# Kernel tuning notes

Measured on AMD Instinct MI355X. Metric: run time of the kernel, lower is better.

## Reference

```python
import jax, jax.numpy as jnp
import numpy as np
from jax import lax

B, C, H, W = 16, 3, 256, 256
K = 3          # lbp kernel size (odd)
POOL = 2
Q = 8          # quant_len
LN_EPS = 1e-5


def _lbp_kernel(c, k):
    half = k // 2
    idx_pairs = [[[0, 0], [k - 1, k - 1]],
                 [[0, half], [k - 1, half]],
                 [[0, k - 1], [k - 1, 0]],
                 [[half, k - 1], [half, 0]]]
    kerns = []
    for pair in idx_pairs:
        for idx in pair:
            m = np.zeros((c, k, k), np.float32)
            m[:, half, half] = 1.0
            m[:, idx[0], idx[1]] = -1.0
            kerns.append(m)
    return jnp.asarray(np.stack(kerns))  # [8, C, K, K]


LBP_KERNEL = _lbp_kernel(C, K)


def setup_inputs() -> dict:
    key = jax.random.key(0)
    ks = jax.random.split(key, 8)
    return {
        "x": jax.random.normal(ks[0], (B, C, H, W), jnp.float32),
        "clamp_low": jnp.float32(-150.0),
        "clamp_high": jnp.float32(150.0),
        "w_expand": jax.random.normal(ks[1], (56, 3, 1, 1), jnp.float32) * 0.1,
        "b_expand": jax.random.normal(ks[2], (56,), jnp.float32) * 0.05,
        "w_conv": jax.random.normal(ks[3], (16, 4, 1, 1), jnp.float32) * 0.1,
        "b_conv": jax.random.normal(ks[4], (16,), jnp.float32) * 0.05,
        "w_final": jax.random.normal(ks[5], (1, 16, 3, 3), jnp.float32) * 0.1,
        "b_final": jax.random.normal(ks[6], (1,), jnp.float32) * 0.05,
    }


def reference(x, clamp_low, clamp_high, w_expand, b_expand, w_conv, b_conv, w_final, b_final):
    leaky = lambda v: jax.nn.leaky_relu(v, 0.01)
    bsz = x.shape[0]

    # avg_pool2d(kernel=POOL, stride=1, pad=POOL//2, count_include_pad=True) -> [B,C,H+1,W+1]
    pad = POOL // 2
    xp = lax.reduce_window(x, 0.0, lax.add, (1, 1, POOL, POOL), (1, 1, 1, 1),
                           [(0, 0), (0, 0), (pad, pad), (pad, pad)]) / float(POOL * POOL)

    # LBP difference conv: 8 output channels, SAME padding
    hk = K // 2
    xl = lax.conv_general_dilated(xp, LBP_KERNEL, (1, 1), [(hk, hk), (hk, hk)],
                                  dimension_numbers=("NCHW", "OIHW", "NCHW"))
    xl = jnp.clip(xl, clamp_low, clamp_high)

    b4 = bsz * 4
    hp, wp = xl.shape[-2], xl.shape[-1]
    n = hp * wp
    xl = xl.reshape(b4, 2, n)  # [B4, 2, N]

    # per-sample, per-channel quantization boundaries: measure[b,i,c] = i*cd + min
    mn = xl.min(axis=-1)                       # [B4, 2]
    mx = xl.max(axis=-1)                       # [B4, 2]
    cd = (mx - mn) / Q
    measure = jnp.arange(Q + 1, dtype=xl.dtype)[None, :, None] * cd[:, None, :] + mn[:, None, :]  # [B4,Q+1,2]

    def bin_mask(vals, ch):
        # keep raw value where lo_i <= v <= hi_i, else 0  -> [B4, Q, N]
        v = vals[:, None, :]
        lo = measure[:, :-1, ch][:, :, None]
        hi = measure[:, 1:, ch][:, :, None]
        return jnp.where((v >= lo) & (v <= hi), v, 0.0)

    m0 = bin_mask(xl[:, 0, :], 0)  # [B4, Q, N]
    m1 = bin_mask(xl[:, 1, :], 1)  # [B4, Q, N]

    # joint histogram of masked values: equivalent to per-pixel outer product + one-hot mask conv
    hist = jnp.einsum("bin,bjn->bij", m0, m1)       # [B4, Q, Q]
    hist = hist / jnp.sum(hist)                      # global normalizer (torch.sum(x))
    hist = hist.reshape(b4, Q * Q, 1)

    # levels: (bin_index + 1) * measure[:, 1, :]
    ii, jj = jnp.meshgrid(jnp.arange(Q), jnp.arange(Q), indexing="ij")
    idxs = jnp.stack([ii, jj], axis=-1).reshape(Q * Q, 2)          # cartesian_prod order
    levels = (idxs[None].astype(xl.dtype) + 1.0) * measure[:, 1, :][:, None, :]  # [B4,64,2]

    feat = jnp.concatenate([levels, hist], axis=2)   # [B4, 64, 3]
    feat = feat.reshape(bsz, 4, Q * Q, 3).transpose(0, 3, 1, 2)  # [B, 3, 4, 64]

    # 1x1 conv 3 -> 56
    h = leaky(jnp.einsum("bcij,oc->boij", feat, w_expand[:, :, 0, 0]) + b_expand[None, :, None, None])
    h = h.transpose(0, 2, 3, 1)  # [B, 4, 64, 56] -> channels=4, spatial (64,56)

    # nearest interpolate spatial (64,56) -> (H,W): src = floor(dst * in / out)
    src_h = (jnp.arange(H) * h.shape[2]) // H
    src_w = (jnp.arange(W) * h.shape[3]) // W
    h = h[:, :, src_h][:, :, :, src_w]  # [B, 4, H, W]

    # layer_norm over last two dims, no affine
    mean = h.mean(axis=(-2, -1), keepdims=True)
    var = jnp.mean((h - mean) ** 2, axis=(-2, -1), keepdims=True)
    h = (h - mean) / jnp.sqrt(var + LN_EPS)

    # 1x1 conv 4 -> 16
    h = leaky(jnp.einsum("bchw,oc->bohw", h, w_conv[:, :, 0, 0]) + b_conv[None, :, None, None])

    # 3x3 conv 16 -> 1, SAME padding
    out = lax.conv_general_dilated(h, w_final, (1, 1), [(1, 1), (1, 1)],
                                   dimension_numbers=("NCHW", "OIHW", "NCHW"))
    out = leaky(out + b_final[None, :, None, None])
    return out
```

## Files before the change

kernel.cpp:

```cpp
#include <hip/hip_runtime.h>
#include <stdint.h>
#include <math.h>

#define HH 256
#define WW 256
#define BATCH 16
#define HP 257
#define SROW 264
#define SB (HP*SROW)
#define NPIX (HP*HP)

__device__ __forceinline__ float leaky(float v){ return v >= 0.f ? v : 0.01f*v; }

__device__ __forceinline__ unsigned fkey(float f){
    unsigned u = __float_as_uint(f);
    return (u & 0x80000000u) ? ~u : (u | 0x80000000u);
}
__device__ __forceinline__ float funkey(unsigned k){
    return (k & 0x80000000u) ? __uint_as_float(k ^ 0x80000000u) : __uint_as_float(~k);
}

__device__ __constant__ int D0H[4] = {-1,-1,-1,0};
__device__ __constant__ int D0W[4] = {-1, 0, 1,1};

__global__ void k1_pool(const float* __restrict__ x, float* __restrict__ s){
    int idx = blockIdx.x*256 + threadIdx.x;
    if (idx >= BATCH*NPIX) return;
    int b = idx / NPIX;
    int r = idx % NPIX;
    int h = r / HP, w = r % HP;
    const float* xb = x + (size_t)b*3*HH*WW;
    float acc = 0.f;
    #pragma unroll
    for (int dy=-1; dy<=0; ++dy){
        int i = h+dy; if ((unsigned)i >= HH) continue;
        #pragma unroll
        for (int dx=-1; dx<=0; ++dx){
            int j = w+dx; if ((unsigned)j >= WW) continue;
            int o = i*WW + j;
            acc += xb[o] + xb[HH*WW + o] + xb[2*HH*WW + o];
        }
    }
    s[(size_t)b*SB + h*SROW + w] = acc * 0.25f;
}

__global__ void k2_minmax(const float* __restrict__ s, const float* __restrict__ cl,
                          const float* __restrict__ chp,
                          unsigned* __restrict__ mnk, unsigned* __restrict__ mxk){
    int g = blockIdx.y;
    int b = g >> 2, k = g & 3;
    int dh = D0H[k], dw = D0W[k];
    float lo = cl[0], hi = chp[0];
    const float* sb = s + (size_t)b*SB;
    float mn0=INFINITY, mx0=-INFINITY, mn1=INFINITY, mx1=-INFINITY;
    for (int idx = blockIdx.x*256 + threadIdx.x; idx < NPIX; idx += gridDim.x*256){
        int h = idx / HP, w = idx % HP;
        float c = sb[h*SROW+w];
        int h0=h+dh, w0=w+dw;
        float n0 = ((unsigned)h0 < HP && (unsigned)w0 < HP) ? sb[h0*SROW+w0] : 0.f;
        int h1=h-dh, w1=w-dw;
        float n1 = ((unsigned)h1 < HP && (unsigned)w1 < HP) ? sb[h1*SROW+w1] : 0.f;
        float v0 = fminf(fmaxf(c-n0, lo), hi);
        float v1 = fminf(fmaxf(c-n1, lo), hi);
        mn0 = fminf(mn0,v0); mx0 = fmaxf(mx0,v0);
        mn1 = fminf(mn1,v1); mx1 = fmaxf(mx1,v1);
    }
    #pragma unroll
    for (int off=32; off; off>>=1){
        mn0 = fminf(mn0, __shfl_down(mn0, off));
        mx0 = fmaxf(mx0, __shfl_down(mx0, off));
        mn1 = fminf(mn1, __shfl_down(mn1, off));
        mx1 = fmaxf(mx1, __shfl_down(mx1, off));
    }
    if ((threadIdx.x & 63) == 0){
        atomicMin(&mnk[g*2+0], fkey(mn0));
        atomicMax(&mxk[g*2+0], fkey(mx0));
        atomicMin(&mnk[g*2+1], fkey(mn1));
        atomicMax(&mxk[g*2+1], fkey(mx1));
    }
}

__global__ void k3_hist(const float* __restrict__ s, const float* __restrict__ cl,
                        const float* __restrict__ chp,
                        const unsigned* __restrict__ mnk, const unsigned* __restrict__ mxk,
                        float* __restrict__ hist){
    __shared__ float lh[8*64];
    int g = blockIdx.y; int b = g>>2, k = g&3;
    int dh = D0H[k], dw = D0W[k];
    float lo = cl[0], hi = chp[0];
    float mn0 = funkey(mnk[g*2+0]), mx0 = funkey(mxk[g*2+0]);
    float mn1 = funkey(mnk[g*2+1]), mx1 = funkey(mxk[g*2+1]);
    float cd0 = (mx0-mn0)*0.125f;
    float cd1 = (mx1-mn1)*0.125f;
    float m0[9], m1[9];
    #pragma unroll
    for (int i=0;i<9;i++){
        m0[i] = __fadd_rn(__fmul_rn((float)i, cd0), mn0);
        m1[i] = __fadd_rn(__fmul_rn((float)i, cd1), mn1);
    }
    for (int t=threadIdx.x; t<512; t+=256) lh[t]=0.f;
    __syncthreads();
    const float* sb = s + (size_t)b*SB;
    int repl = (threadIdx.x & 7) * 64;
    for (int idx = blockIdx.x*256 + threadIdx.x; idx < NPIX; idx += gridDim.x*256){
        int h = idx/HP, w = idx%HP;
        float c = sb[h*SROW+w];
        int h0=h+dh, w0=w+dw;
        float n0 = ((unsigned)h0<HP && (unsigned)w0<HP) ? sb[h0*SROW+w0] : 0.f;
        int h1=h-dh, w1=w-dw;
        float n1 = ((unsigned)h1<HP && (unsigned)w1<HP) ? sb[h1*SROW+w1] : 0.f;
        float v0 = fminf(fmaxf(c-n0, lo), hi);
        float v1 = fminf(fmaxf(c-n1, lo), hi);
        unsigned b0=0, b1=0;
        #pragma unroll
        for (int i=0;i<8;i++){
            b0 |= (v0>=m0[i] && v0<=m0[i+1]) ? (1u<<i) : 0u;
            b1 |= (v1>=m1[i] && v1<=m1[i+1]) ? (1u<<i) : 0u;
        }
        float p = v0*v1;
        unsigned bb0=b0;
        while (bb0){
            int i = __ffs(bb0)-1; bb0 &= bb0-1;
            unsigned bb1=b1;
            while (bb1){
                int j = __ffs(bb1)-1; bb1 &= bb1-1;
                atomicAdd(&lh[repl + i*8 + j], p);
            }
        }
    }
    __syncthreads();
    if (threadIdx.x < 64){
        float acc=0.f;
        #pragma unroll
        for (int r=0;r<8;r++) acc += lh[r*64+threadIdx.x];
        atomicAdd(&hist[g*64+threadIdx.x], acc);
    }
}

__global__ void k4a(const float* __restrict__ hist,
                    const unsigned* __restrict__ mnk, const unsigned* __restrict__ mxk,
                    const float* __restrict__ we, const float* __restrict__ be,
                    float* __restrict__ hsm, float* __restrict__ stats){
    __shared__ float hloc[3584];
    __shared__ float sred[4];
    int g = blockIdx.x;
    int tid = threadIdx.x;
    float ps = 0.f;
    for (int t=tid; t<4096; t+=256) ps += hist[t];
    #pragma unroll
    for (int off=32; off; off>>=1) ps += __shfl_down(ps, off);
    if ((tid&63)==0) sred[tid>>6] = ps;
    __syncthreads();
    float S = sred[0]+sred[1]+sred[2]+sred[3];

    float mn0 = funkey(mnk[g*2+0]), mx0 = funkey(mxk[g*2+0]);
    float mn1 = funkey(mnk[g*2+1]), mx1 = funkey(mxk[g*2+1]);
    float lvl0 = __fadd_rn((mx0-mn0)*0.125f, mn0);
    float lvl1 = __fadd_rn((mx1-mn1)*0.125f, mn1);

    for (int e=tid; e<3584; e+=256){
        int ij = e/56, o = e%56;
        int i = ij>>3, j = ij&7;
        float f0 = __fmul_rn((float)(i+1), lvl0);
        float f1 = __fmul_rn((float)(j+1), lvl1);
        float f2 = hist[g*64+ij] / S;
        float a = f0*we[o*3+0] + f1*we[o*3+1] + f2*we[o*3+2] + be[o];
        a = leaky(a);
        hloc[e] = a;
        hsm[(size_t)g*3584 + e] = a;
    }
    __syncthreads();

    float pm = 0.f;
    for (int e=tid; e<3584; e+=256){
        int o = e%56;
        int lo_ = (32*o+6)/7, hi_ = (32*o+31)/7;
        float wgt = (float)(4*(hi_-lo_+1));
        pm += hloc[e]*wgt;
    }
    #pragma unroll
    for (int off=32; off; off>>=1) pm += __shfl_down(pm, off);
    if ((tid&63)==0) sred[tid>>6]=pm;
    __syncthreads();
    float mean = (sred[0]+sred[1]+sred[2]+sred[3]) * (1.0f/65536.0f);
    __syncthreads();
    float pv = 0.f;
    for (int e=tid; e<3584; e+=256){
        int o = e%56;
        int lo_ = (32*o+6)/7, hi_ = (32*o+31)/7;
        float wgt = (float)(4*(hi_-lo_+1));
        float d = hloc[e]-mean;
        pv += d*d*wgt;
    }
    #pragma unroll
    for (int off=32; off; off>>=1) pv += __shfl_down(pv, off);
    if ((tid&63)==0) sred[tid>>6]=pv;
    __syncthreads();
    float var = (sred[0]+sred[1]+sred[2]+sred[3]) * (1.0f/65536.0f);
    if (tid==0){
        stats[g*2+0] = mean;
        stats[g*2+1] = 1.0f / sqrtf(var + 1e-5f);
    }
}

__global__ void k4b(const float* __restrict__ hsm, const float* __restrict__ stats,
                    const float* __restrict__ wc, const float* __restrict__ bc,
                    float* __restrict__ hcv){
    int idx = blockIdx.x*256+threadIdx.x;
    if (idx >= 16*64*56*16) return;
    int c = idx & 15;
    int t = idx >> 4;
    int o = t % 56; t /= 56;
    int ij = t & 63; int b = t >> 6;
    float acc = bc[c];
    #pragma unroll
    for (int k=0;k<4;k++){
        int g = b*4+k;
        float hv = hsm[(size_t)g*3584 + ij*56 + o];
        float hn = (hv - stats[g*2])*stats[g*2+1];
        acc += wc[c*4+k]*hn;
    }
    hcv[idx] = leaky(acc);
}

__global__ void k5a(const float* __restrict__ hcv, const float* __restrict__ wf,
                    float* __restrict__ F){
    __shared__ float wfl[144];
    if (threadIdx.x < 144) wfl[threadIdx.x] = wf[threadIdx.x];
    __syncthreads();
    int idx = blockIdx.x*256+threadIdx.x;
    if (idx >= 16*256*56) return;
    int sxc = idx % 56;
    int y = (idx/56) & 255;
    int b = idx / (56*256);
    float f0=0.f, f1=0.f, f2=0.f;
    #pragma unroll
    for (int dy=0; dy<3; ++dy){
        int yy = y + dy - 1;
        if ((unsigned)yy >= 256) continue;
        int r = yy >> 2;
        const float* hc = hcv + (((size_t)b*64 + r)*56 + sxc)*16;
        #pragma unroll
        for (int c=0;c<16;c++){
            float hv = hc[c];
            f0 += wfl[c*9 + dy*3 + 0]*hv;
            f1 += wfl[c*9 + dy*3 + 1]*hv;
            f2 += wfl[c*9 + dy*3 + 2]*hv;
        }
    }
    float* Fb = F + (((size_t)b*256 + y)*3)*56;
    Fb[0*56+sxc]=f0; Fb[1*56+sxc]=f1; Fb[2*56+sxc]=f2;
}

__global__ void k5b(const float* __restrict__ F, const float* __restrict__ bf,
                    float* __restrict__ out){
    int idx = blockIdx.x*256+threadIdx.x;
    if (idx >= 16*256*256) return;
    int x = idx & 255;
    int y = (idx >> 8) & 255;
    int b = idx >> 16;
    float acc = bf[0];
    const float* Fb = F + ((size_t)b*256 + y)*3*56;
    #pragma unroll
    for (int dx=0; dx<3; ++dx){
        int xx = x + dx - 1;
        if ((unsigned)xx >= 256) continue;
        int sxx = (xx*7) >> 5;
        acc += Fb[dx*56 + sxx];
    }
    out[idx] = leaky(acc);
}

extern "C" void kernel_launch(void* const* d_in, const int* in_sizes, int n_in,
                              void* d_out, int out_size, void* d_ws, size_t ws_size,
                              hipStream_t stream){
    const float* x  = (const float*)d_in[0];
    const float* cl = (const float*)d_in[1];
    const float* ch = (const float*)d_in[2];
    const float* we = (const float*)d_in[3];
    const float* be = (const float*)d_in[4];
    const float* wc = (const float*)d_in[5];
    const float* bc = (const float*)d_in[6];
    const float* wf = (const float*)d_in[7];
    const float* bf = (const float*)d_in[8];
    float* out = (float*)d_out;

    float* s = (float*)d_ws;
    size_t off = (size_t)16*SB;
    unsigned* mnk = (unsigned*)(s + off); off += 128;
    unsigned* mxk = (unsigned*)(s + off); off += 128;
    float* hist = s + off; off += 4096;
    float* hsm  = s + off; off += 229376;
    float* stats= s + off; off += 128;
    float* hcv  = s + off; off += 917504;
    float* F    = s;

    hipMemsetAsync(mnk, 0xFF, 128*4, stream);
    hipMemsetAsync(mxk, 0x00, 128*4, stream);
    hipMemsetAsync(hist, 0, 4096*4, stream);

    k1_pool<<<dim3((BATCH*NPIX+255)/256), 256, 0, stream>>>(x, s);
    k2_minmax<<<dim3(8,64), 256, 0, stream>>>(s, cl, ch, mnk, mxk);
    k3_hist<<<dim3(16,64), 256, 0, stream>>>(s, cl, ch, mnk, mxk, hist);
    k4a<<<64, 256, 0, stream>>>(hist, mnk, mxk, we, be, hsm, stats);
    k4b<<<(16*64*56*16+255)/256, 256, 0, stream>>>(hsm, stats, wc, bc, hcv);
    k5a<<<(16*256*56+255)/256, 256, 0, stream>>>(hcv, wf, F);
    k5b<<<(16*256*256+255)/256, 256, 0, stream>>>(F, bf, out);
}
```

Measured before the change: 163.4 us.

## Pad pooled image, fuse memsets and tail convs, group LBP directions per block

The pooled image is stored with a zero halo so the neighbour lookups in the min/max and histogram kernels need no bounds checks. Each block's four wavefronts now handle the four direction groups of one sample. The three memsets are folded into the pool kernel. The 1x1 conv and the vertical 3x3 weighting are fused into one kernel that emits per-tap partial sums at low resolution, and a single output kernel gathers them, replacing three kernels. This cuts launch count and the intermediate traffic for hcv and F, at the cost of a more intricate tap decomposition that relies on nearest-neighbour replication.

```diff
diff --git a/kernel.cpp b/kernel.cpp
--- a/kernel.cpp
+++ b/kernel.cpp
@@ -7,7 +7,8 @@
 #define BATCH 16
 #define HP 257
 #define SROW 264
-#define SB (HP*SROW)
+#define SH 259
+#define SBP (SH*SROW)
 #define NPIX (HP*HP)
 
 __device__ __forceinline__ float leaky(float v){ return v >= 0.f ? v : 0.01f*v; }
@@ -20,48 +21,59 @@
     return (k & 0x80000000u) ? __uint_as_float(k ^ 0x80000000u) : __uint_as_float(~k);
 }
 
-__device__ __constant__ int D0H[4] = {-1,-1,-1,0};
-__device__ __constant__ int D0W[4] = {-1, 0, 1,1};
-
-__global__ void k1_pool(const float* __restrict__ x, float* __restrict__ s){
+__device__ __forceinline__ void group_off(int k, int& dh, int& dw){
+    dh = (k == 3) ? 0 : -1;
+    dw = (k == 3) ? 1 : (k - 1);
+}
+
+__global__ __launch_bounds__(256) void k1_pool(const float* __restrict__ x, float* __restrict__ s,
+                                               unsigned* __restrict__ mnk, unsigned* __restrict__ mxk,
+                                               float* __restrict__ hist){
+    if (blockIdx.x == 0){
+        if (threadIdx.x < 128){ mnk[threadIdx.x] = 0xFFFFFFFFu; mxk[threadIdx.x] = 0u; }
+        for (int t = threadIdx.x; t < 4096; t += 256) hist[t] = 0.f;
+    }
     int idx = blockIdx.x*256 + threadIdx.x;
-    if (idx >= BATCH*NPIX) return;
-    int b = idx / NPIX;
-    int r = idx % NPIX;
-    int h = r / HP, w = r % HP;
-    const float* xb = x + (size_t)b*3*HH*WW;
-    float acc = 0.f;
-    #pragma unroll
-    for (int dy=-1; dy<=0; ++dy){
-        int i = h+dy; if ((unsigned)i >= HH) continue;
+    if (idx >= BATCH*SBP) return;
+    int b = idx / SBP;
+    int r = idx % SBP;
+    int ph = r / SROW, pw = r % SROW;
+    int h = ph - 1, w = pw - 1;
+    float val = 0.f;
+    if ((unsigned)h < (unsigned)HP && (unsigned)w < (unsigned)HP){
+        const float* xb = x + (size_t)b*3*HH*WW;
+        float acc = 0.f;
         #pragma unroll
-        for (int dx=-1; dx<=0; ++dx){
-            int j = w+dx; if ((unsigned)j >= WW) continue;
-            int o = i*WW + j;
-            acc += xb[o] + xb[HH*WW + o] + xb[2*HH*WW + o];
+        for (int dy=-1; dy<=0; ++dy){
+            int i = h+dy; if ((unsigned)i >= HH) continue;
+            #pragma unroll
+            for (int dx=-1; dx<=0; ++dx){
+                int j = w+dx; if ((unsigned)j >= WW) continue;
+                int o = i*WW + j;
+                acc += xb[o] + xb[HH*WW + o] + xb[2*HH*WW + o];
+            }
         }
-    }
-    s[(size_t)b*SB + h*SROW + w] = acc * 0.25f;
-}
-
-__global__ void k2_minmax(const float* __restrict__ s, const float* __restrict__ cl,
-                          const float* __restrict__ chp,
-                          unsigned* __restrict__ mnk, unsigned* __restrict__ mxk){
-    int g = blockIdx.y;
-    int b = g >> 2, k = g & 3;
-    int dh = D0H[k], dw = D0W[k];
+        val = acc * 0.25f;
+    }
+    s[idx] = val;
+}
+
+__global__ __launch_bounds__(256) void k2_minmax(const float* __restrict__ s, const float* __restrict__ cl,
+                                                 const float* __restrict__ chp,
+                                                 unsigned* __restrict__ mnk, unsigned* __restrict__ mxk){
+    int b = blockIdx.y;
+    int wv = threadIdx.x >> 6, lane = threadIdx.x & 63;
+    int dh, dw; group_off(wv, dh, dw);
+    int doff = dh*SROW + dw;
     float lo = cl[0], hi = chp[0];
-    const float* sb = s + (size_t)b*SB;
+    const float* sp = s + (size_t)b*SBP + SROW + 1;
     float mn0=INFINITY, mx0=-INFINITY, mn1=INFINITY, mx1=-INFINITY;
-    for (int idx = blockIdx.x*256 + threadIdx.x; idx < NPIX; idx += gridDim.x*256){
-        int h = idx / HP, w = idx % HP;
-        float c = sb[h*SROW+w];
-        int h0=h+dh, w0=w+dw;
-        float n0 = ((unsigned)h0 < HP && (unsigned)w0 < HP) ? sb[h0*SROW+w0] : 0.f;
-        int h1=h-dh, w1=w-dw;
-        float n1 = ((unsigned)h1 < HP && (unsigned)w1 < HP) ? sb[h1*SROW+w1] : 0.f;
-        float v0 = fminf(fmaxf(c-n0, lo), hi);
-        float v1 = fminf(fmaxf(c-n1, lo), hi);
+    for (int idx = blockIdx.x*64 + lane; idx < NPIX; idx += gridDim.x*64){
+        int h = idx / HP, w = idx - h*HP;
+        const float* p = sp + h*SROW + w;
+        float c = p[0];
+        float v0 = fminf(fmaxf(c - p[doff],  lo), hi);
+        float v1 = fminf(fmaxf(c - p[-doff], lo), hi);
         mn0 = fminf(mn0,v0); mx0 = fmaxf(mx0,v0);
         mn1 = fminf(mn1,v1); mx1 = fmaxf(mx1,v1);
     }
@@ -72,7 +84,8 @@
         mn1 = fminf(mn1, __shfl_down(mn1, off));
         mx1 = fmaxf(mx1, __shfl_down(mx1, off));
     }
-    if ((threadIdx.x & 63) == 0){
+    if (lane == 0){
+        int g = b*4 + wv;
         atomicMin(&mnk[g*2+0], fkey(mn0));
         atomicMax(&mxk[g*2+0], fkey(mx0));
         atomicMin(&mnk[g*2+1], fkey(mn1));
@@ -80,13 +93,16 @@
     }
 }
 
-__global__ void k3_hist(const float* __restrict__ s, const float* __restrict__ cl,
-                        const float* __restrict__ chp,
-                        const unsigned* __restrict__ mnk, const unsigned* __restrict__ mxk,
-                        float* __restrict__ hist){
-    __shared__ float lh[8*64];
-    int g = blockIdx.y; int b = g>>2, k = g&3;
-    int dh = D0H[k], dw = D0W[k];
+__global__ __launch_bounds__(256) void k3_hist(const float* __restrict__ s, const float* __restrict__ cl,
+                                               const float* __restrict__ chp,
+                                               const unsigned* __restrict__ mnk, const unsigned* __restrict__ mxk,
+                                               float* __restrict__ hist){
+    __shared__ float lh[4*64*8];
+    int b = blockIdx.y;
+    int wv = threadIdx.x >> 6, lane = threadIdx.x & 63;
+    for (int t = threadIdx.x; t < 2048; t += 256) lh[t] = 0.f;
+    __syncthreads();
+    int g = b*4 + wv;
     float lo = cl[0], hi = chp[0];
     float mn0 = funkey(mnk[g*2+0]), mx0 = funkey(mxk[g*2+0]);
     float mn1 = funkey(mnk[g*2+1]), mx1 = funkey(mxk[g*2+1]);
@@ -98,46 +114,42 @@
         m0[i] = __fadd_rn(__fmul_rn((float)i, cd0), mn0);
         m1[i] = __fadd_rn(__fmul_rn((float)i, cd1), mn1);
     }
-    for (int t=threadIdx.x; t<512; t+=256) lh[t]=0.f;
-    __syncthreads();
-    const float* sb = s + (size_t)b*SB;
-    int repl = (threadIdx.x & 7) * 64;
-    for (int idx = blockIdx.x*256 + threadIdx.x; idx < NPIX; idx += gridDim.x*256){
-        int h = idx/HP, w = idx%HP;
-        float c = sb[h*SROW+w];
-        int h0=h+dh, w0=w+dw;
-        float n0 = ((unsigned)h0<HP && (unsigned)w0<HP) ? sb[h0*SROW+w0] : 0.f;
-        int h1=h-dh, w1=w-dw;
-        float n1 = ((unsigned)h1<HP && (unsigned)w1<HP) ? sb[h1*SROW+w1] : 0.f;
-        float v0 = fminf(fmaxf(c-n0, lo), hi);
-        float v1 = fminf(fmaxf(c-n1, lo), hi);
+    int dh, dw; group_off(wv, dh, dw);
+    int doff = dh*SROW + dw;
+    const float* sp = s + (size_t)b*SBP + SROW + 1;
+    float* lhg = lh + wv*512 + (lane & 7);
+    for (int idx = blockIdx.x*64 + lane; idx < NPIX; idx += gridDim.x*64){
+        int h = idx / HP, w = idx - h*HP;
+        const float* p = sp + h*SROW + w;
+        float c = p[0];
+        float v0 = fminf(fmaxf(c - p[doff],  lo), hi);
+        float v1 = fminf(fmaxf(c - p[-doff], lo), hi);
         unsigned b0=0, b1=0;
         #pragma unroll
         for (int i=0;i<8;i++){
             b0 |= (v0>=m0[i] && v0<=m0[i+1]) ? (1u<<i) : 0u;
             b1 |= (v1>=m1[i] && v1<=m1[i+1]) ? (1u<<i) : 0u;
         }
-        float p = v0*v1;
+        float pr = v0*v1;
         unsigned bb0=b0;
         while (bb0){
             int i = __ffs(bb0)-1; bb0 &= bb0-1;
             unsigned bb1=b1;
             while (bb1){
                 int j = __ffs(bb1)-1; bb1 &= bb1-1;
-                atomicAdd(&lh[repl + i*8 + j], p);
+                atomicAdd(&lhg[(i*8+j)*8], pr);
             }
         }
     }
     __syncthreads();
-    if (threadIdx.x < 64){
-        float acc=0.f;
-        #pragma unroll
-        for (int r=0;r<8;r++) acc += lh[r*64+threadIdx.x];
-        atomicAdd(&hist[g*64+threadIdx.x], acc);
-    }
-}
-
-__global__ void k4a(const float* __restrict__ hist,
+    int gg = threadIdx.x >> 6, bin = threadIdx.x & 63;
+    float acc = 0.f;
+    #pragma unroll
+    for (int r=0;r<8;r++) acc += lh[gg*512 + bin*8 + r];
+    atomicAdd(&hist[(b*4+gg)*64 + bin], acc);
+}
+
+__global__ __launch_bounds__(256) void k4a(const float* __restrict__ hist,
                     const unsigned* __restrict__ mnk, const unsigned* __restrict__ mxk,
                     const float* __restrict__ we, const float* __restrict__ be,
                     float* __restrict__ hsm, float* __restrict__ stats){
@@ -155,8 +167,8 @@
 
     float mn0 = funkey(mnk[g*2+0]), mx0 = funkey(mxk[g*2+0]);
     float mn1 = funkey(mnk[g*2+1]), mx1 = funkey(mxk[g*2+1]);
-    float lvl0 = __fadd_rn((mx0-mn0)*0.125f, mn0);
-    float lvl1 = __fadd_rn((mx1-mn1)*0.125f, mn1);
+    float lvl0 = __fadd_rn(__fmul_rn(1.0f,(mx0-mn0)*0.125f), mn0);
+    float lvl1 = __fadd_rn(__fmul_rn(1.0f,(mx1-mn1)*0.125f), mn1);
 
     for (int e=tid; e<3584; e+=256){
         int ij = e/56, o = e%56;
@@ -203,72 +215,60 @@
     }
 }
 
-__global__ void k4b(const float* __restrict__ hsm, const float* __restrict__ stats,
-                    const float* __restrict__ wc, const float* __restrict__ bc,
-                    float* __restrict__ hcv){
-    int idx = blockIdx.x*256+threadIdx.x;
-    if (idx >= 16*64*56*16) return;
-    int c = idx & 15;
-    int t = idx >> 4;
-    int o = t % 56; t /= 56;
-    int ij = t & 63; int b = t >> 6;
-    float acc = bc[c];
+__global__ __launch_bounds__(256) void k4w(const float* __restrict__ hsm, const float* __restrict__ stats,
+                                           const float* __restrict__ wc, const float* __restrict__ bc,
+                                           const float* __restrict__ wf,
+                                           float* __restrict__ w9g){
+    __shared__ float wfl[144];
+    if (threadIdx.x < 144) wfl[threadIdx.x] = wf[threadIdx.x];
+    __syncthreads();
+    int idx = blockIdx.x*256 + threadIdx.x;
+    if (idx >= 16*64*56) return;
+    int sxc = idx % 56;
+    int r = (idx/56) & 63;
+    int b = idx / (56*64);
+    int e = r*56 + sxc;
+    float hn[4];
     #pragma unroll
     for (int k=0;k<4;k++){
         int g = b*4+k;
-        float hv = hsm[(size_t)g*3584 + ij*56 + o];
-        float hn = (hv - stats[g*2])*stats[g*2+1];
-        acc += wc[c*4+k]*hn;
-    }
-    hcv[idx] = leaky(acc);
-}
-
-__global__ void k5a(const float* __restrict__ hcv, const float* __restrict__ wf,
-                    float* __restrict__ F){
-    __shared__ float wfl[144];
-    if (threadIdx.x < 144) wfl[threadIdx.x] = wf[threadIdx.x];
-    __syncthreads();
-    int idx = blockIdx.x*256+threadIdx.x;
-    if (idx >= 16*256*56) return;
-    int sxc = idx % 56;
-    int y = (idx/56) & 255;
-    int b = idx / (56*256);
-    float f0=0.f, f1=0.f, f2=0.f;
+        hn[k] = (hsm[(size_t)g*3584 + e] - stats[g*2]) * stats[g*2+1];
+    }
+    float w9v[9] = {0,0,0,0,0,0,0,0,0};
+    #pragma unroll
+    for (int c=0;c<16;c++){
+        float hv = bc[c];
+        #pragma unroll
+        for (int k=0;k<4;k++) hv += wc[c*4+k]*hn[k];
+        hv = leaky(hv);
+        #pragma unroll
+        for (int t=0;t<9;t++) w9v[t] += wfl[c*9+t]*hv;
+    }
+    float* dst = w9g + (((size_t)b*64 + r)*9)*56 + sxc;
+    #pragma unroll
+    for (int t=0;t<9;t++) dst[t*56] = w9v[t];
+}
+
+__global__ __launch_bounds__(256) void k5_out(const float* __restrict__ w9g, const float* __restrict__ bf,
+                                              float* __restrict__ out){
+    int x = threadIdx.x;
+    int y = blockIdx.x & 255;
+    int b = blockIdx.x >> 8;
+    const float* wb = w9g + (size_t)b*64*9*56;
+    float acc = bf[0];
+    int sxm = ((x-1)*7) >> 5;
+    int sx0 = (x*7) >> 5;
+    int sxp = ((x+1)*7) >> 5;
     #pragma unroll
     for (int dy=0; dy<3; ++dy){
         int yy = y + dy - 1;
-        if ((unsigned)yy >= 256) continue;
-        int r = yy >> 2;
-        const float* hc = hcv + (((size_t)b*64 + r)*56 + sxc)*16;
-        #pragma unroll
-        for (int c=0;c<16;c++){
-            float hv = hc[c];
-            f0 += wfl[c*9 + dy*3 + 0]*hv;
-            f1 += wfl[c*9 + dy*3 + 1]*hv;
-            f2 += wfl[c*9 + dy*3 + 2]*hv;
-        }
-    }
-    float* Fb = F + (((size_t)b*256 + y)*3)*56;
-    Fb[0*56+sxc]=f0; Fb[1*56+sxc]=f1; Fb[2*56+sxc]=f2;
-}
-
-__global__ void k5b(const float* __restrict__ F, const float* __restrict__ bf,
-                    float* __restrict__ out){
-    int idx = blockIdx.x*256+threadIdx.x;
-    if (idx >= 16*256*256) return;
-    int x = idx & 255;
-    int y = (idx >> 8) & 255;
-    int b = idx >> 16;
-    float acc = bf[0];
-    const float* Fb = F + ((size_t)b*256 + y)*3*56;
-    #pragma unroll
-    for (int dx=0; dx<3; ++dx){
-        int xx = x + dx - 1;
-        if ((unsigned)xx >= 256) continue;
-        int sxx = (xx*7) >> 5;
-        acc += Fb[dx*56 + sxx];
-    }
-    out[idx] = leaky(acc);
+        if ((unsigned)yy >= 256u) continue;
+        const float* wr = wb + (((yy>>2)*9) + dy*3)*56;
+        if (x >= 1)   acc += wr[0*56 + sxm];
+                      acc += wr[1*56 + sx0];
+        if (x <= 254) acc += wr[2*56 + sxp];
+    }
+    out[((size_t)(b*256 + y))*256 + x] = leaky(acc);
 }
 
 extern "C" void kernel_launch(void* const* d_in, const int* in_sizes, int n_in,
@@ -286,24 +286,18 @@
     float* out = (float*)d_out;
 
     float* s = (float*)d_ws;
-    size_t off = (size_t)16*SB;
+    size_t off = (size_t)BATCH*SBP;
     unsigned* mnk = (unsigned*)(s + off); off += 128;
     unsigned* mxk = (unsigned*)(s + off); off += 128;
     float* hist = s + off; off += 4096;
     float* hsm  = s + off; off += 229376;
     float* stats= s + off; off += 128;
-    float* hcv  = s + off; off += 917504;
-    float* F    = s;
-
-    hipMemsetAsync(mnk, 0xFF, 128*4, stream);
-    hipMemsetAsync(mxk, 0x00, 128*4, stream);
-    hipMemsetAsync(hist, 0, 4096*4, stream);
-
-    k1_pool<<<dim3((BATCH*NPIX+255)/256), 256, 0, stream>>>(x, s);
-    k2_minmax<<<dim3(8,64), 256, 0, stream>>>(s, cl, ch, mnk, mxk);
-    k3_hist<<<dim3(16,64), 256, 0, stream>>>(s, cl, ch, mnk, mxk, hist);
+    float* w9g  = s + off; off += (size_t)16*64*9*56;
+
+    k1_pool<<<(BATCH*SBP + 255)/256, 256, 0, stream>>>(x, s, mnk, mxk, hist);
+    k2_minmax<<<dim3(32,16), 256, 0, stream>>>(s, cl, ch, mnk, mxk);
+    k3_hist<<<dim3(16,16), 256, 0, stream>>>(s, cl, ch, mnk, mxk, hist);
     k4a<<<64, 256, 0, stream>>>(hist, mnk, mxk, we, be, hsm, stats);
-    k4b<<<(16*64*56*16+255)/256, 256, 0, stream>>>(hsm, stats, wc, bc, hcv);
-    k5a<<<(16*256*56+255)/256, 256, 0, stream>>>(hcv, wf, F);
-    k5b<<<(16*256*256+255)/256, 256, 0, stream>>>(F, bf, out);
-}
+    k4w<<<(16*64*56 + 255)/256, 256, 0, stream>>>(hsm, stats, wc, bc, wf, w9g);
+    k5_out<<<16*256, 256, 0, stream>>>(w9g, bf, out);
+}
```

After: 162.5 us. No clear change (-0.6%).
